# Performance work log

Hardware: AMD Instinct MI355X
Metric: run time of the kernel (lower is better)

The kernel has to match this reference:

```python
import jax, jax.numpy as jnp
import numpy as np

NEG_INF = -9e15
ALPHA = 0.2  # LeakyReLU negative slope
OUT_FEATURES = 128


def setup_inputs() -> dict:
    key = jax.random.key(0)
    k1, k2, k3, k4 = jax.random.split(key, 4)
    B, N, F_in, F_out = 4, 4096, 256, OUT_FEATURES
    h = jax.random.normal(k1, (B, N, F_in), dtype=jnp.float32)
    adj = jax.random.randint(k2, (B, N, N), 0, 2, dtype=jnp.int32)
    W = jax.random.normal(k3, (F_in, F_out), dtype=jnp.float32) * 0.07
    a = jax.random.normal(k4, (2 * F_out, 1), dtype=jnp.float32) * 0.1
    return {"h": h, "adj": adj, "W": W, "a": a}


def reference(h, adj, W, a):
    # Wh: (B, N, F_out)
    Wh = jnp.einsum('bni,io->bno', h, W)
    a1 = a[:OUT_FEATURES, 0]   # (F_out,)
    a2 = a[OUT_FEATURES:, 0]   # (F_out,)
    Wh1 = Wh @ a1              # (B, N)
    Wh2 = Wh @ a2              # (B, N)
    e = Wh1[:, :, None] + Wh2[:, None, :]          # (B, N, N)
    e = jnp.where(e >= 0, e, ALPHA * e)             # LeakyReLU
    e = jnp.where(adj > 0, e, NEG_INF)              # adjacency mask
    attention = jax.nn.softmax(e, axis=-1)          # (B, N, N)
    # dropout omitted: reference runs in eval mode (training=False)
    h_prime = jnp.einsum('bnm,bmo->bno', attention, Wh)
    return jax.nn.elu(h_prime)  # concat=True
```

## Files before the change

### kernel.cpp

```cpp
#include <hip/hip_runtime.h>
#include <hip/hip_bf16.h>
#include <math.h>

typedef __attribute__((ext_vector_type(4))) float  f32x4;
typedef __attribute__((ext_vector_type(4))) int    i32x4;
typedef __attribute__((ext_vector_type(8))) short  s16x8;
typedef __attribute__((ext_vector_type(4))) short  s16x4;
typedef __attribute__((ext_vector_type(8))) __bf16 bf16x8;

#define LOG2E 1.4426950408889634f

__device__ __forceinline__ short f32_to_bf16_rne(float f) {
    unsigned u = __builtin_bit_cast(unsigned, f);
    u += 0x7fffu + ((u >> 16) & 1u);
    return (short)(u >> 16);
}
__device__ __forceinline__ int pack2_bf16(float f0, float f1) {
    unsigned u0 = __builtin_bit_cast(unsigned, f0) + 0x8000u;
    unsigned u1 = __builtin_bit_cast(unsigned, f1) + 0x8000u;
    return (int)((u0 >> 16) | (u1 & 0xffff0000u));
}
__device__ __forceinline__ bf16x8 as_bf16x8(s16x8 v) {
    return __builtin_bit_cast(bf16x8, v);
}
__device__ __forceinline__ bf16x8 as_bf16x8(i32x4 v) {
    return __builtin_bit_cast(bf16x8, v);
}

__global__ void k0_wt(const float* __restrict__ W, short* __restrict__ WT) {
    int g = blockIdx.x * 256 + threadIdx.x;
    int col = g >> 6;
    int k0 = (g & 63) * 4;
    s16x4 v;
    #pragma unroll
    for (int i = 0; i < 4; ++i) v[i] = f32_to_bf16_rne(W[(k0 + i) * 128 + col]);
    *(s16x4*)(WT + col * 256 + k0) = v;
}

__global__ __launch_bounds__(256, 2) void k1_gemm(
    const float* __restrict__ h, const float* __restrict__ a,
    const short* __restrict__ WT,
    short* __restrict__ WhT, float* __restrict__ Wh1p, float* __restrict__ Tp)
{
    int l = threadIdx.x & 63;
    int w = threadIdx.x >> 6;
    int gw = blockIdx.x * 4 + w;
    int r0 = gw * 16;
    int lm = l & 15, q = l >> 4;

    f32x4 acc[8];
    #pragma unroll
    for (int ct = 0; ct < 8; ++ct) acc[ct] = (f32x4)0.0f;

    const float* hrow = h + (long)(r0 + lm) * 256;
    for (int kb = 0; kb < 8; ++kb) {
        int kbase = kb * 32 + q * 8;
        f32x4 h0 = *(const f32x4*)(hrow + kbase);
        f32x4 h1 = *(const f32x4*)(hrow + kbase + 4);
        s16x8 af;
        #pragma unroll
        for (int j = 0; j < 4; ++j) af[j] = f32_to_bf16_rne(h0[j]);
        #pragma unroll
        for (int j = 0; j < 4; ++j) af[4 + j] = f32_to_bf16_rne(h1[j]);
        bf16x8 afb = as_bf16x8(af);
        #pragma unroll
        for (int ct = 0; ct < 8; ++ct) {
            s16x8 bf = *(const s16x8*)(WT + (ct * 16 + lm) * 256 + kbase);
            acc[ct] = __builtin_amdgcn_mfma_f32_16x16x32_bf16(afb, as_bf16x8(bf), acc[ct], 0, 0, 0);
        }
    }

    int b = r0 >> 12;
    int nb = r0 & 4095;
    float p1[4] = {0.f, 0.f, 0.f, 0.f}, p2[4] = {0.f, 0.f, 0.f, 0.f};
    #pragma unroll
    for (int ct = 0; ct < 8; ++ct) {
        int col = ct * 16 + lm;
        float a1c = a[col], a2c = a[128 + col];
        s16x4 vv;
        #pragma unroll
        for (int r = 0; r < 4; ++r) {
            float v = acc[ct][r];
            p1[r] += v * a1c;
            p2[r] += v * a2c;
            vv[r] = f32_to_bf16_rne(v);
        }
        *(s16x4*)(WhT + ((long)(b * 128 + col) * 4096 + nb + q * 4)) = vv;
    }
    #pragma unroll
    for (int off = 1; off < 16; off <<= 1) {
        #pragma unroll
        for (int r = 0; r < 4; ++r) {
            p1[r] += __shfl_xor(p1[r], off);
            p2[r] += __shfl_xor(p2[r], off);
        }
    }
    if (lm == 0) {
        #pragma unroll
        for (int r = 0; r < 4; ++r) {
            int row = r0 + q * 4 + r;
            Wh1p[row] = LOG2E * p1[r];
            Tp[row]   = LOG2E * p2[r];
        }
    }
}

__global__ void k2_tmax(const float* __restrict__ Tp, float* __restrict__ Tmax) {
    __shared__ float red[256];
    int b = blockIdx.x, t = threadIdx.x;
    float mx = -1e30f;
    for (int i = 0; i < 16; ++i) mx = fmaxf(mx, Tp[b * 4096 + t + i * 256]);
    red[t] = mx;
    __syncthreads();
    for (int s = 128; s > 0; s >>= 1) {
        if (t < s) red[t] = fmaxf(red[t], red[t + s]);
        __syncthreads();
    }
    if (t == 0) Tmax[b] = red[0];
}

template <int SPLIT>
__global__ __launch_bounds__(256, 2) void k3_attn(
    const int* __restrict__ adj, const short* __restrict__ WhT,
    const float* __restrict__ Wh1p, const float* __restrict__ Tp,
    const float* __restrict__ Tmax,
    float* __restrict__ U, float* __restrict__ Z)
{
    const int MSLICE = 4096 / SPLIT;
    const int MTILES = MSLICE / 128;
    __shared__ __align__(16) short tile[2][128 * 128];
    __shared__ __align__(16) float tps[4096 / SPLIT];

    int l = threadIdx.x & 63, w = threadIdx.x >> 6;
    int lm = l & 15, q = l >> 4;
    int bid = blockIdx.x;
    int p8 = bid & (4 * SPLIT - 1);
    int b  = p8 / SPLIT;
    int mh = p8 % SPLIT;
    int rg = bid / (4 * SPLIT);
    int n0 = rg * 64;
    int mbase = mh * MSLICE;

    int n_lane = n0 + w * 16 + lm;
    float sp = Wh1p[b * 4096 + n_lane];
    float xm = sp + Tmax[b];
    float Mrow = fmaxf(xm, 0.2f * xm);

    const int*   adjrow = adj + ((long)(b * 4096 + n_lane) << 12) + q * 8;
    const short* whtb   = WhT + (long)b * 128 * 4096;
    const float* tpsq   = tps + q * 8;

    {
        const float* tg = Tp + b * 4096 + mbase;
        int i0 = threadIdx.x * 4;
        *(f32x4*)(tps + i0)        = *(const f32x4*)(tg + i0);
        *(f32x4*)(tps + i0 + 1024) = *(const f32x4*)(tg + i0 + 1024);
    }

    f32x4 acc[8];
    #pragma unroll
    for (int ct = 0; ct < 8; ++ct) acc[ct] = (f32x4)0.0f;
    float z = 0.0f;

    auto stage = [&](short* dst, int m0) {
        int colw = w * 32;
        #pragma unroll
        for (int j = 0; j < 8; ++j) {
            int cb = colw + j * 4;
            int col = cb + q;
            int gch = lm ^ (col & 7);
            const short* gp = whtb + (long)col * 4096 + m0 + gch * 8;
            __builtin_amdgcn_global_load_lds(
                (const __attribute__((address_space(1))) void*)gp,
                (__attribute__((address_space(3))) void*)(dst + cb * 128), 16, 0, 0);
        }
    };
    auto ldadj = [&](i32x4* aj, int m0) {
        #pragma unroll
        for (int ks = 0; ks < 4; ++ks) {
            aj[2 * ks]     = *(const i32x4*)(adjrow + m0 + ks * 32);
            aj[2 * ks + 1] = *(const i32x4*)(adjrow + m0 + ks * 32 + 4);
        }
    };
    auto compute = [&](const short* buf, const i32x4* aj, int mrel) {
        #pragma unroll
        for (int ks = 0; ks < 4; ++ks) {
            f32x4 t0 = *(const f32x4*)(tpsq + mrel + ks * 32);
            f32x4 t1 = *(const f32x4*)(tpsq + mrel + ks * 32 + 4);
            i32x4 pk;
            float zs = 0.0f;
            #pragma unroll
            for (int half = 0; half < 2; ++half) {
                i32x4 a4 = aj[2 * ks + half];
                f32x4 t4 = half ? t1 : t0;
                float wv[4];
                #pragma unroll
                for (int j = 0; j < 4; ++j) {
                    float y = sp + t4[j];
                    float e = fmaxf(y, 0.2f * y) - Mrow;
                    float v = __builtin_amdgcn_exp2f(e);
                    v = (a4[j] != 0) ? v : 0.0f;
                    zs += v; wv[j] = v;
                }
                pk[half * 2]     = pack2_bf16(wv[0], wv[1]);
                pk[half * 2 + 1] = pack2_bf16(wv[2], wv[3]);
            }
            z += zs;
            bf16x8 ab = as_bf16x8(pk);
            #pragma unroll
            for (int ct = 0; ct < 8; ++ct) {
                int col = ct * 16 + lm;
                int pos = (ks * 4 + q) ^ (col & 7);
                s16x8 bf = *(const s16x8*)(buf + col * 128 + pos * 8);
                acc[ct] = __builtin_amdgcn_mfma_f32_16x16x32_bf16(ab, as_bf16x8(bf), acc[ct], 0, 0, 0);
            }
        }
    };

    #define SUBPHASE(CBUF, SBUF, AJ_LD, AJ_USE, TC, TS, TA)                    \
        stage(SBUF, mbase + ((TS) & (MTILES - 1)) * 128);                      \
        __builtin_amdgcn_sched_barrier(0);                                     \
        ldadj(AJ_LD, mbase + ((TA) & (MTILES - 1)) * 128);                     \
        __builtin_amdgcn_sched_barrier(0);                                     \
        asm volatile("s_waitcnt vmcnt(24)" ::: "memory");                      \
        __builtin_amdgcn_s_barrier();                                          \
        __builtin_amdgcn_sched_barrier(0);                                     \
        compute(CBUF, AJ_USE, (TC) * 128);                                     \
        __builtin_amdgcn_sched_barrier(0);                                     \
        __builtin_amdgcn_s_barrier();                                          \
        __builtin_amdgcn_sched_barrier(0);

    i32x4 ajA[8], ajB[8], ajC[8], ajD[8];
    stage(tile[0], mbase);
    __builtin_amdgcn_sched_barrier(0);
    ldadj(ajA, mbase);
    ldadj(ajB, mbase + 128);
    __builtin_amdgcn_sched_barrier(0);
    asm volatile("s_waitcnt vmcnt(0) lgkmcnt(0)" ::: "memory");
    __builtin_amdgcn_s_barrier();
    __builtin_amdgcn_sched_barrier(0);

    #pragma unroll 1
    for (int t = 0; t < MTILES; t += 4) {
        SUBPHASE(tile[0], tile[1], ajC, ajA, t,     t + 1, t + 2)
        SUBPHASE(tile[1], tile[0], ajD, ajB, t + 1, t + 2, t + 3)
        SUBPHASE(tile[0], tile[1], ajA, ajC, t + 2, t + 3, t + 4)
        SUBPHASE(tile[1], tile[0], ajB, ajD, t + 3, t + 4, t + 5)
    }
    #undef SUBPHASE

    z += __shfl_xor(z, 16);
    z += __shfl_xor(z, 32);

    int slice = b * SPLIT + mh;
    if (l < 16) Z[slice * 4096 + n0 + w * 16 + lm] = z;
    float* ub = U + ((long)slice * 4096 + n0 + w * 16) * 128;
    #pragma unroll
    for (int ct = 0; ct < 8; ++ct) {
        int col = ct * 16 + lm;
        #pragma unroll
        for (int r = 0; r < 4; ++r)
            ub[(q * 4 + r) * 128 + col] = acc[ct][r];
    }
}

__global__ void k4_combine(const float* __restrict__ U, const float* __restrict__ Z,
                           float* __restrict__ out) {
    long g = (long)blockIdx.x * 256 + threadIdx.x;
    long off = g * 4;
    long nf = off >> 7;
    int b = (int)(nf >> 12), n = (int)(nf & 4095), col = (int)(off & 127);
    long base0 = ((long)(b * 2) * 4096 + n) * 128 + col;
    f32x4 u0 = *(const f32x4*)(U + base0);
    f32x4 u1 = *(const f32x4*)(U + base0 + (long)4096 * 128);
    float zz = Z[(b * 2) * 4096 + n] + Z[(b * 2 + 1) * 4096 + n];
    f32x4 v;
    #pragma unroll
    for (int i = 0; i < 4; ++i) {
        float x = (u0[i] + u1[i]) / zz;
        v[i] = (x > 0.f) ? x : (expf(x) - 1.0f);
    }
    *(f32x4*)(out + off) = v;
}

extern "C" void kernel_launch(void* const* d_in, const int* in_sizes, int n_in,
                              void* d_out, int out_size, void* d_ws, size_t ws_size,
                              hipStream_t stream) {
    const float* h   = (const float*)d_in[0];
    const int*   adj = (const int*)d_in[1];
    const float* W   = (const float*)d_in[2];
    const float* a   = (const float*)d_in[3];
    float* out = (float*)d_out;

    char* ws = (char*)d_ws;
    short* WhT  = (short*)ws;
    short* WT   = (short*)(ws + 4194304);
    float* Wh1p = (float*)(ws + 4259840);
    float* Tp   = (float*)(ws + 4325376);
    float* Tmax = (float*)(ws + 4390912);
    float* U    = (float*)(ws + 4391168);
    float* Z    = (float*)(ws + 4391168 + 16777216);

    k0_wt<<<32, 256, 0, stream>>>(W, WT);
    k1_gemm<<<256, 256, 0, stream>>>(h, a, WT, WhT, Wh1p, Tp);
    k2_tmax<<<4, 256, 0, stream>>>(Tp, Tmax);
    k3_attn<2><<<512, 256, 0, stream>>>(adj, WhT, Wh1p, Tp, Tmax, U, Z);
    k4_combine<<<2048, 256, 0, stream>>>(U, Z, out);
    (void)in_sizes; (void)n_in; (void)out_size; (void)ws_size;
}
```

Baseline: 415.5 us.

## Load adjacency row-coalesced and share it as LDS bitmasks across lanes

Each wave now reads adjacency with lanes spanning contiguous columns (8-byte loads per row over 16 rows), which coalesces better than the old per-lane strided 16-byte row loads. The values are packed into 32-bit bitmasks in LDS and read back in the MFMA operand layout during compute. The goal is higher effective bandwidth on the int32 adjacency stream, which dominates memory traffic. The cost is more load instructions in flight (waitcnt raised to 40), extra pack ALU work, and LDS traffic, and it relies on the existing barrier to order LDS writes and reads.

```diff
diff --git a/kernel.cpp b/kernel.cpp
--- a/kernel.cpp
+++ b/kernel.cpp
@@ -4,6 +4,7 @@
 
 typedef __attribute__((ext_vector_type(4))) float  f32x4;
 typedef __attribute__((ext_vector_type(4))) int    i32x4;
+typedef __attribute__((ext_vector_type(2))) int    i32x2;
 typedef __attribute__((ext_vector_type(8))) short  s16x8;
 typedef __attribute__((ext_vector_type(4))) short  s16x4;
 typedef __attribute__((ext_vector_type(8))) __bf16 bf16x8;
@@ -130,6 +131,7 @@
     const int MTILES = MSLICE / 128;
     __shared__ __align__(16) short tile[2][128 * 128];
     __shared__ __align__(16) float tps[4096 / SPLIT];
+    __shared__ __align__(16) unsigned bmw[4][64];
 
     int l = threadIdx.x & 63, w = threadIdx.x >> 6;
     int lm = l & 15, q = l >> 4;
@@ -146,9 +148,9 @@
     float xm = sp + Tmax[b];
     float Mrow = fmaxf(xm, 0.2f * xm);
 
-    const int*   adjrow = adj + ((long)(b * 4096 + n_lane) << 12) + q * 8;
-    const short* whtb   = WhT + (long)b * 128 * 4096;
-    const float* tpsq   = tps + q * 8;
+    const short* whtb = WhT + (long)b * 128 * 4096;
+    const float* tpsq = tps + q * 8;
+    const int* adjb = adj + ((long)(b * 4096 + n0 + w * 16) << 12) + mbase + l * 2;
 
     {
         const float* tg = Tp + b * 4096 + mbase;
@@ -156,6 +158,9 @@
         *(f32x4*)(tps + i0)        = *(const f32x4*)(tg + i0);
         *(f32x4*)(tps + i0 + 1024) = *(const f32x4*)(tg + i0 + 1024);
     }
+    asm volatile("s_waitcnt vmcnt(0) lgkmcnt(0)" ::: "memory");
+    __builtin_amdgcn_s_barrier();
+    __builtin_amdgcn_sched_barrier(0);
 
     f32x4 acc[8];
     #pragma unroll
@@ -175,23 +180,30 @@
                 (__attribute__((address_space(3))) void*)(dst + cb * 128), 16, 0, 0);
         }
     };
-    auto ldadj = [&](i32x4* aj, int m0) {
+    auto ldadj = [&](i32x2* R, int m0) {
+        #pragma unroll
+        for (int r = 0; r < 16; ++r)
+            R[r] = *(const i32x2*)(adjb + ((long)r << 12) + m0);
+    };
+    auto pack = [&](const i32x2* R) {
+        unsigned P = 0;
+        #pragma unroll
+        for (int r = 0; r < 16; ++r) {
+            if (R[r][0] != 0) P |= (1u << (2 * r));
+            if (R[r][1] != 0) P |= (1u << (2 * r + 1));
+        }
+        bmw[w][l] = P;
+    };
+    auto compute = [&](const short* buf, int mrel) {
         #pragma unroll
         for (int ks = 0; ks < 4; ++ks) {
-            aj[2 * ks]     = *(const i32x4*)(adjrow + m0 + ks * 32);
-            aj[2 * ks + 1] = *(const i32x4*)(adjrow + m0 + ks * 32 + 4);
-        }
-    };
-    auto compute = [&](const short* buf, const i32x4* aj, int mrel) {
-        #pragma unroll
-        for (int ks = 0; ks < 4; ++ks) {
+            i32x4 bw = *(const i32x4*)&bmw[w][16 * ks + 4 * q];
             f32x4 t0 = *(const f32x4*)(tpsq + mrel + ks * 32);
             f32x4 t1 = *(const f32x4*)(tpsq + mrel + ks * 32 + 4);
             i32x4 pk;
             float zs = 0.0f;
             #pragma unroll
             for (int half = 0; half < 2; ++half) {
-                i32x4 a4 = aj[2 * ks + half];
                 f32x4 t4 = half ? t1 : t0;
                 float wv[4];
                 #pragma unroll
@@ -199,7 +211,8 @@
                     float y = sp + t4[j];
                     float e = fmaxf(y, 0.2f * y) - Mrow;
                     float v = __builtin_amdgcn_exp2f(e);
-                    v = (a4[j] != 0) ? v : 0.0f;
+                    unsigned word = (unsigned)bw[2 * half + (j >> 1)];
+                    v = ((word >> (2 * lm + (j & 1))) & 1u) ? v : 0.0f;
                     zs += v; wv[j] = v;
                 }
                 pk[half * 2]     = pack2_bf16(wv[0], wv[1]);
@@ -217,35 +230,36 @@
         }
     };
 
-    #define SUBPHASE(CBUF, SBUF, AJ_LD, AJ_USE, TC, TS, TA)                    \
+    #define SUBPHASE(CBUF, SBUF, R_LD, R_USE, TC, TS, TA)                      \
         stage(SBUF, mbase + ((TS) & (MTILES - 1)) * 128);                      \
         __builtin_amdgcn_sched_barrier(0);                                     \
-        ldadj(AJ_LD, mbase + ((TA) & (MTILES - 1)) * 128);                     \
-        __builtin_amdgcn_sched_barrier(0);                                     \
-        asm volatile("s_waitcnt vmcnt(24)" ::: "memory");                      \
+        ldadj(R_LD, ((TA) & (MTILES - 1)) * 128);                              \
+        __builtin_amdgcn_sched_barrier(0);                                     \
+        asm volatile("s_waitcnt vmcnt(40)" ::: "memory");                      \
+        __builtin_amdgcn_sched_barrier(0);                                     \
+        pack(R_USE);                                                           \
+        __builtin_amdgcn_sched_barrier(0);                                     \
         __builtin_amdgcn_s_barrier();                                          \
         __builtin_amdgcn_sched_barrier(0);                                     \
-        compute(CBUF, AJ_USE, (TC) * 128);                                     \
+        compute(CBUF, (TC) * 128);                                             \
         __builtin_amdgcn_sched_barrier(0);                                     \
         __builtin_amdgcn_s_barrier();                                          \
         __builtin_amdgcn_sched_barrier(0);
 
-    i32x4 ajA[8], ajB[8], ajC[8], ajD[8];
+    i32x2 RA[16], RB[16], RC[16], RD[16];
     stage(tile[0], mbase);
     __builtin_amdgcn_sched_barrier(0);
-    ldadj(ajA, mbase);
-    ldadj(ajB, mbase + 128);
+    ldadj(RA, 0);
     __builtin_amdgcn_sched_barrier(0);
-    asm volatile("s_waitcnt vmcnt(0) lgkmcnt(0)" ::: "memory");
-    __builtin_amdgcn_s_barrier();
+    ldadj(RB, 128);
     __builtin_amdgcn_sched_barrier(0);
 
     #pragma unroll 1
     for (int t = 0; t < MTILES; t += 4) {
-        SUBPHASE(tile[0], tile[1], ajC, ajA, t,     t + 1, t + 2)
-        SUBPHASE(tile[1], tile[0], ajD, ajB, t + 1, t + 2, t + 3)
-        SUBPHASE(tile[0], tile[1], ajA, ajC, t + 2, t + 3, t + 4)
-        SUBPHASE(tile[1], tile[0], ajB, ajD, t + 3, t + 4, t + 5)
+        SUBPHASE(tile[0], tile[1], RC, RA, t,     t + 1, t + 2)
+        SUBPHASE(tile[1], tile[0], RD, RB, t + 1, t + 2, t + 3)
+        SUBPHASE(tile[0], tile[1], RA, RC, t + 2, t + 3, t + 4)
+        SUBPHASE(tile[1], tile[0], RB, RD, t + 3, t + 4, t + 5)
     }
     #undef SUBPHASE
 
```

Measured after the change: 444.7 us. +7.0%, slower.
